# Kernel tuning notes

Hardware: AMD Instinct MI355X
Metric: run time of the kernel (lower is better)

The kernel has to match this reference:

```python
import jax, jax.numpy as jnp
import numpy as np

B, S, E, H = 2, 2048, 4096, 32
D = E // H  # head_dim = 128
MAX_SEQ = 2048


def precompute_freqs(dim, end, theta=10000.0):
    # Faithful to the torch source, including its operator precedence:
    # freqs = 1.0 / (theta ** arange(0, dim, 2)[:dim//2].float() / dim)
    # i.e. 1.0 / ((theta ** exps) / dim); overflows to inf in fp32 -> freq 0.
    exps = jnp.arange(0, dim, 2, dtype=jnp.float32)[: dim // 2]
    freqs = 1.0 / (jnp.power(jnp.float32(theta), exps) / jnp.float32(dim))
    t = jnp.arange(end, dtype=jnp.float32)
    f = jnp.outer(t, freqs)  # [end, dim//2]
    return jnp.cos(f), jnp.sin(f)


def apply_rope(x, cos, sin, pos):
    # x: [B,H,S,D]; cos/sin: [max_seq, dim//2]; pos: [B,S]
    c = cos[pos][:, None]  # [B,1,S,f]
    s = sin[pos][:, None]
    xr = x.reshape(*x.shape[:-1], -1, 2)  # [B,H,S,D/2,2]
    x1, x2 = xr[..., 0], xr[..., 1]
    if x1.shape[-1] > c.shape[-1]:
        rep = x1.shape[-1] // c.shape[-1]  # repeat_interleave factor
        c = jnp.repeat(c, rep, axis=-1)
        s = jnp.repeat(s, rep, axis=-1)
    out = jnp.stack([x1 * c - x2 * s, x1 * s + x2 * c], axis=-1)
    return out.reshape(x.shape)


def setup_inputs() -> dict:
    key = jax.random.key(0)
    kx, kq, kk, kv, ko = jax.random.split(key, 5)
    x = jax.random.normal(kx, (B, S, E), jnp.float32)
    scale = 0.02
    Wq = jax.random.normal(kq, (E, E), jnp.float32) * scale
    Wk = jax.random.normal(kk, (E, E), jnp.float32) * scale
    Wv = jax.random.normal(kv, (E, E), jnp.float32) * scale
    Wo = jax.random.normal(ko, (E, E), jnp.float32) * scale
    z = jnp.zeros((E,), jnp.float32)
    return {"x": x, "Wq": Wq, "bq": z, "Wk": Wk, "bk": z, "Wv": Wv, "bv": z, "Wo": Wo, "bo": z}


def reference(x, Wq, bq, Wk, bk, Wv, bv, Wo, bo):
    cos, sin = precompute_freqs(H, MAX_SEQ)  # note: dim = n_heads, as in source
    pos = jnp.broadcast_to(jnp.arange(S)[None, :], (B, S))  # no offset, S <= max
    # QKV projections (torch Linear: x @ W.T + b)
    q = (x @ Wq.T + bq).reshape(B, S, H, D).transpose(0, 2, 1, 3)  # [B,H,S,D]
    k = (x @ Wk.T + bk).reshape(B, S, H, D).transpose(0, 2, 1, 3)
    v = (x @ Wv.T + bv).reshape(B, S, H, D).transpose(0, 2, 1, 3)
    q = apply_rope(q, cos, sin, pos)
    k = apply_rope(k, cos, sin, pos)
    # SDPA with mask=None (non-causal, full attention)
    scores = jnp.einsum("bhqd,bhkd->bhqk", q, k) / np.float32(np.sqrt(D))
    att = jax.nn.softmax(scores, axis=-1)
    out = jnp.einsum("bhqk,bhkd->bhqd", att, v)
    out = out.transpose(0, 2, 1, 3).reshape(B, S, E)
    return out @ Wo.T + bo
```

## Files before the change

kernel.cpp:

```cpp
#include <hip/hip_runtime.h>
#include <math.h>

typedef _Float16 half8 __attribute__((ext_vector_type(8)));
typedef float f32x4 __attribute__((ext_vector_type(4)));

struct FreqT { float f[16]; };

__device__ __forceinline__ f32x4 mfma16(half8 a, half8 b, f32x4 c) {
  return __builtin_amdgcn_mfma_f32_16x16x32_f16(a, b, c, 0, 0, 0);
}

__device__ __forceinline__ void gload_lds16(const void* g, void* l) {
  __builtin_amdgcn_global_load_lds(
      (const __attribute__((address_space(1))) void*)g,
      (__attribute__((address_space(3))) void*)l, 16, 0, 0);
}

#define S_BARRIER() __builtin_amdgcn_s_barrier()
#define WAIT_LGKM0() asm volatile("s_waitcnt lgkmcnt(0)" ::: "memory")
#define WAIT_VM8() asm volatile("s_waitcnt vmcnt(8)" ::: "memory")
#define WAIT_VM0() asm volatile("s_waitcnt vmcnt(0)" ::: "memory")

__global__ __launch_bounds__(256)
void cast_f32_f16(const float* __restrict__ in, _Float16* __restrict__ out, long n8) {
  long i = (long)blockIdx.x * blockDim.x + threadIdx.x;
  if (i >= n8) return;
  float4 a = ((const float4*)in)[2 * i];
  float4 b = ((const float4*)in)[2 * i + 1];
  half8 v;
  v[0] = (_Float16)a.x; v[1] = (_Float16)a.y; v[2] = (_Float16)a.z; v[3] = (_Float16)a.w;
  v[4] = (_Float16)b.x; v[5] = (_Float16)b.y; v[6] = (_Float16)b.z; v[7] = (_Float16)b.w;
  ((half8*)out)[i] = v;
}

#define GBM 256
#define GBN 256
#define GBK 64

template <typename OutT>
__global__ __launch_bounds__(512, 2)
void gemm256(const _Float16* __restrict__ A, const _Float16* __restrict__ W,
             const float* __restrict__ bias, OutT* __restrict__ C,
             int M, int N, int K) {
  __shared__ __align__(16) _Float16 lds[4][GBM * GBK];

  int nwg = gridDim.x;
  int bid = blockIdx.x;
  int cpx = nwg >> 3;
  int swz = (bid & 7) * cpx + (bid >> 3);
  int ntn = N / GBN;
  int m0 = (swz / ntn) * GBM, n0 = (swz % ntn) * GBN;

  int tid = threadIdx.x, lane = tid & 63, w = tid >> 6;
  int wm = w >> 2, wn = w & 3;
  int g = lane >> 4, lc = lane & 15;

  int r8 = w * 8 + (lane >> 3);
  int cs = (((lane & 7) ^ (lane >> 3)) << 3);
  const _Float16* gA = A + (size_t)(m0 + r8) * K + cs;
  const _Float16* gB = W + (size_t)(n0 + r8) * K + cs;

#define STAGE(bi, k0) do {                                            \
    _Float16* la_ = &lds[(bi) * 2][0] + w * 512;                      \
    _Float16* lb_ = &lds[(bi) * 2 + 1][0] + w * 512;                  \
    _Pragma("unroll")                                                 \
    for (int i_ = 0; i_ < 4; ++i_) {                                  \
      gload_lds16(gA + (size_t)(i_ * 64) * K + (k0), la_ + i_ * 4096);\
      gload_lds16(gB + (size_t)(i_ * 64) * K + (k0), lb_ + i_ * 4096);\
    } } while (0)

  int aOff[8], bOff[4];
#pragma unroll
  for (int mf = 0; mf < 8; ++mf) aOff[mf] = (wm * 128 + mf * 16 + lc) * 64;
#pragma unroll
  for (int nf = 0; nf < 4; ++nf) bOff[nf] = (wn * 64 + nf * 16 + lc) * 64;
  int co0 = (((0 * 4 + g) ^ (lc & 7)) << 3);
  int co1 = (((1 * 4 + g) ^ (lc & 7)) << 3);

  half8 a0[8], a1[8], b0[4], b1[4];
  f32x4 acc[8][4] = {};

#define LOAD_SET0(bi) do {                                            \
    const _Float16* lA_ = &lds[(bi) * 2][0];                          \
    const _Float16* lB_ = &lds[(bi) * 2 + 1][0];                      \
    _Pragma("unroll")                                                 \
    for (int mf = 0; mf < 4; ++mf) {                                  \
      a0[mf * 2 + 0] = *(const half8*)&lA_[aOff[mf] + co0];           \
      a0[mf * 2 + 1] = *(const half8*)&lA_[aOff[mf] + co1];           \
    }                                                                 \
    _Pragma("unroll")                                                 \
    for (int nf = 0; nf < 2; ++nf) {                                  \
      b0[nf * 2 + 0] = *(const half8*)&lB_[bOff[nf] + co0];           \
      b0[nf * 2 + 1] = *(const half8*)&lB_[bOff[nf] + co1];           \
    } } while (0)

#define LOAD_SET1(bi) do {                                            \
    const _Float16* lA_ = &lds[(bi) * 2][0];                          \
    const _Float16* lB_ = &lds[(bi) * 2 + 1][0];                      \
    _Pragma("unroll")                                                 \
    for (int mf = 0; mf < 4; ++mf) {                                  \
      a1[mf * 2 + 0] = *(const half8*)&lA_[aOff[mf + 4] + co0];       \
      a1[mf * 2 + 1] = *(const half8*)&lA_[aOff[mf + 4] + co1];       \
    }                                                                 \
    _Pragma("unroll")                                                 \
    for (int nf = 0; nf < 2; ++nf) {                                  \
      b1[nf * 2 + 0] = *(const half8*)&lB_[bOff[nf + 2] + co0];       \
      b1[nf * 2 + 1] = *(const half8*)&lB_[bOff[nf + 2] + co1];       \
    } } while (0)

#define MFMA_Q(mq, nq, ar, br) do {                                   \
    __builtin_amdgcn_s_setprio(1);                                    \
    _Pragma("unroll")                                                 \
    for (int mf = 0; mf < 4; ++mf)                                    \
      _Pragma("unroll")                                               \
      for (int nf = 0; nf < 2; ++nf)                                  \
        _Pragma("unroll")                                             \
        for (int kk = 0; kk < 2; ++kk)                                \
          acc[(mq) * 4 + mf][(nq) * 2 + nf] =                         \
              mfma16(ar[mf * 2 + kk], br[nf * 2 + kk],                \
                     acc[(mq) * 4 + mf][(nq) * 2 + nf]);              \
    __builtin_amdgcn_s_setprio(0); } while (0)

  const int NT = K >> 6;

  STAGE(0, 0);
  STAGE(1, GBK);
  WAIT_VM8();
  S_BARRIER();
  LOAD_SET0(0);

  for (int t = 0; t < NT - 2; ++t) {
    int cur = t & 1;
    LOAD_SET1(cur);
    MFMA_Q(0, 0, a0, b0);
    MFMA_Q(0, 1, a0, b1);
    WAIT_LGKM0();
    S_BARRIER();
    STAGE(cur, (t + 2) << 6);
    MFMA_Q(1, 1, a1, b1);
    MFMA_Q(1, 0, a1, b0);
    WAIT_VM8();
    S_BARRIER();
    LOAD_SET0(cur ^ 1);
  }
  {
    int cur = (NT - 2) & 1;
    LOAD_SET1(cur);
    MFMA_Q(0, 0, a0, b0);
    MFMA_Q(0, 1, a0, b1);
    MFMA_Q(1, 1, a1, b1);
    MFMA_Q(1, 0, a1, b0);
    WAIT_VM0();
    S_BARRIER();
    LOAD_SET0(cur ^ 1);
  }
  {
    int cur = (NT - 1) & 1;
    LOAD_SET1(cur);
    MFMA_Q(0, 0, a0, b0);
    MFMA_Q(0, 1, a0, b1);
    MFMA_Q(1, 1, a1, b1);
    MFMA_Q(1, 0, a1, b0);
  }

  int crow = m0 + wm * 128 + g * 4;
  int ccol = n0 + wn * 64 + lc;
#pragma unroll
  for (int nf = 0; nf < 4; ++nf) {
    float bv = bias[ccol + nf * 16];
#pragma unroll
    for (int mf = 0; mf < 8; ++mf)
#pragma unroll
      for (int j = 0; j < 4; ++j)
        C[(size_t)(crow + mf * 16 + j) * N + ccol + nf * 16] =
            (OutT)(acc[mf][nf][j] + bv);
  }
#undef STAGE
#undef LOAD_SET0
#undef LOAD_SET1
#undef MFMA_Q
}

__global__ __launch_bounds__(256)
void rope_kernel(_Float16* __restrict__ x, FreqT ft, int Sn, int E, long n8) {
  long i = (long)blockIdx.x * blockDim.x + threadIdx.x;
  if (i >= n8) return;
  int epr = E / 8;
  int e8 = (int)(i % epr);
  int s = (int)((i / epr) % Sn);
  int fj = e8 & 15;
  float fr = ft.f[fj];
  float ang = (float)s * fr;
  float sv, cv;
  sincosf(ang, &sv, &cv);
  half8 v = ((const half8*)x)[i];
  half8 o;
#pragma unroll
  for (int p = 0; p < 4; ++p) {
    float x1 = (float)v[2 * p], x2 = (float)v[2 * p + 1];
    o[2 * p] = (_Float16)(x1 * cv - x2 * sv);
    o[2 * p + 1] = (_Float16)(x1 * sv + x2 * cv);
  }
  ((half8*)x)[i] = o;
}

#define QB 128
#define KB 64

__global__ __launch_bounds__(256)
void flash_attn(const _Float16* __restrict__ qg, const _Float16* __restrict__ kg,
                const _Float16* __restrict__ vg, _Float16* __restrict__ og,
                int Bn, int Hn, int Sn) {
  const int D = 128;
  const int E = Hn * D;

  __shared__ _Float16 Ksh[KB * 128];
  __shared__ _Float16 Vsh[128 * 64];
  __shared__ _Float16 Psh[4 * 32 * 64];

  int qtiles = Sn / QB;
  int bid = blockIdx.x;
  int bh = bid / qtiles, qt = bid % qtiles;
  int b = bh / Hn, h = bh % Hn;

  int tid = threadIdx.x, lane = tid & 63, w = tid >> 6;
  int g = lane >> 4, lc = lane & 15;
  int lc7 = lc & 7;

  const size_t headoff = ((size_t)b * Sn) * E + (size_t)h * D;
  const _Float16* qp = qg + headoff;
  const _Float16* kp = kg + headoff;
  const _Float16* vp = vg + headoff;

  int q0 = qt * QB + w * 32;
  half8 aq[2][4];
#pragma unroll
  for (int mf = 0; mf < 2; ++mf)
#pragma unroll
    for (int kf = 0; kf < 4; ++kf)
      aq[mf][kf] = *(const half8*)(qp + (size_t)(q0 + mf * 16 + lc) * E + kf * 32 + g * 8);

  float mrun[2][4], lpart[2][4];
  f32x4 o[2][8] = {};
#pragma unroll
  for (int mf = 0; mf < 2; ++mf)
#pragma unroll
    for (int j = 0; j < 4; ++j) { mrun[mf][j] = -1e30f; lpart[mf][j] = 0.f; }

  const float scale = 0.08838834764831845f;

  int krow = 4 * w + (lane >> 4);
  int kcol = ((lane & 15) ^ (krow & 7)) * 8;
  const _Float16* gK = kp + (size_t)krow * E + kcol;
  _Float16* lK = Ksh + w * 512;

  half8 vreg[4];
#pragma unroll
  for (int p = 0; p < 4; ++p)
    vreg[p] = *(const half8*)(vp + (size_t)lane * E + p * 32 + w * 8);

  int kvlo = lane & 7, kvhi = lane >> 3;
  _Float16* Pw = Psh + w * 2048;

  const int NT = Sn / KB;
  for (int kt = 0; kt < NT; ++kt) {
    __syncthreads();
#pragma unroll
    for (int i = 0; i < 4; ++i)
      gload_lds16(gK + (size_t)(kt * KB + 16 * i) * E, lK + i * 2048);
#pragma unroll
    for (int p = 0; p < 4; ++p) {
      int d0 = p * 32 + w * 8;
#pragma unroll
      for (int i = 0; i < 8; ++i)
        Vsh[(d0 + i) * 64 + (kvlo | (((kvhi ^ i) & 7) << 3))] = vreg[p][i];
    }
    __syncthreads();

    f32x4 s[2][4] = {};
    __builtin_amdgcn_s_setprio(1);
#pragma unroll
    for (int kf = 0; kf < 4; ++kf) {
      half8 bk[4];
#pragma unroll
      for (int nf = 0; nf < 4; ++nf)
        bk[nf] = *(const half8*)&Ksh[(nf * 16 + lc) * 128 + (((kf * 4 + g) ^ lc7) << 3)];
#pragma unroll
      for (int mf = 0; mf < 2; ++mf)
#pragma unroll
        for (int nf = 0; nf < 4; ++nf)
          s[mf][nf] = mfma16(aq[mf][kf], bk[nf], s[mf][nf]);
    }
    __builtin_amdgcn_s_setprio(0);

#pragma unroll
    for (int mf = 0; mf < 2; ++mf) {
      f32x4 mx = s[mf][0];
#pragma unroll
      for (int nf = 1; nf < 4; ++nf)
#pragma unroll
        for (int j = 0; j < 4; ++j) mx[j] = fmaxf(mx[j], s[mf][nf][j]);
#pragma unroll
      for (int d = 1; d < 16; d <<= 1)
#pragma unroll
        for (int j = 0; j < 4; ++j) mx[j] = fmaxf(mx[j], __shfl_xor(mx[j], d));
      bool need = false;
#pragma unroll
      for (int j = 0; j < 4; ++j) need |= (mx[j] * scale > mrun[mf][j] + 8.f);
      if (__any(need)) {
#pragma unroll
        for (int j = 0; j < 4; ++j) {
          float mnew = fmaxf(mrun[mf][j], mx[j] * scale);
          float r = __expf(mrun[mf][j] - mnew);
          mrun[mf][j] = mnew;
          lpart[mf][j] *= r;
#pragma unroll
          for (int df = 0; df < 8; ++df) o[mf][df][j] *= r;
        }
      }
#pragma unroll
      for (int nf = 0; nf < 4; ++nf) {
        int colbase = nf * 16 + lc;
        int chi = colbase >> 3, clo = colbase & 7;
#pragma unroll
        for (int j = 0; j < 4; ++j) {
          float p = __expf(s[mf][nf][j] * scale - mrun[mf][j]);
          lpart[mf][j] += p;
          int row = mf * 16 + g * 4 + j;
          Pw[row * 64 + (clo | (((chi ^ (row & 7)) & 7) << 3))] = (_Float16)p;
        }
      }
    }

    if (kt + 1 < NT) {
#pragma unroll
      for (int p = 0; p < 4; ++p)
        vreg[p] = *(const half8*)(vp + (size_t)((kt + 1) * KB + lane) * E + p * 32 + w * 8);
    }

    __builtin_amdgcn_s_setprio(1);
#pragma unroll
    for (int kk = 0; kk < 2; ++kk) {
      half8 ap0 = *(const half8*)&Pw[lc * 64 + (((kk * 4 + g) ^ lc7) << 3)];
      half8 ap1 = *(const half8*)&Pw[(16 + lc) * 64 + (((kk * 4 + g) ^ lc7) << 3)];
#pragma unroll
      for (int df = 0; df < 8; ++df) {
        half8 bv = *(const half8*)&Vsh[(df * 16 + lc) * 64 + (((kk * 4 + g) ^ lc7) << 3)];
        o[0][df] = mfma16(ap0, bv, o[0][df]);
        o[1][df] = mfma16(ap1, bv, o[1][df]);
      }
    }
    __builtin_amdgcn_s_setprio(0);
  }

  _Float16* op = og + headoff;
#pragma unroll
  for (int mf = 0; mf < 2; ++mf) {
#pragma unroll
    for (int j = 0; j < 4; ++j) {
      float l = lpart[mf][j];
#pragma unroll
      for (int d = 1; d < 16; d <<= 1) l += __shfl_xor(l, d);
      float inv = 1.0f / l;
      int row = q0 + mf * 16 + g * 4 + j;
#pragma unroll
      for (int df = 0; df < 8; ++df)
        op[(size_t)row * E + df * 16 + lc] = (_Float16)(o[mf][df][j] * inv);
    }
  }
}

extern "C" void kernel_launch(void* const* d_in, const int* in_sizes, int n_in,
                              void* d_out, int out_size, void* d_ws, size_t ws_size,
                              hipStream_t stream) {
  const float* x  = (const float*)d_in[0];
  const float* Wq = (const float*)d_in[1];
  const float* bq = (const float*)d_in[2];
  const float* Wk = (const float*)d_in[3];
  const float* bk = (const float*)d_in[4];
  const float* Wv = (const float*)d_in[5];
  const float* bv = (const float*)d_in[6];
  const float* Wo = (const float*)d_in[7];
  const float* bo = (const float*)d_in[8];

  const int E = in_sizes[2];
  const int M = in_sizes[0] / E;
  const int S = 2048;
  const int Bb = M / S;
  const int H = 32;

  _Float16* xh = (_Float16*)d_ws;
  _Float16* wh = xh + (size_t)M * E;
  _Float16* qh = wh + (size_t)E * E;
  _Float16* kh = qh + (size_t)M * E;
  _Float16* vh = kh + (size_t)M * E;
  _Float16* oh = xh;

  FreqT ft;
  for (int j = 0; j < 16; ++j) {
    float pf = (float)pow(10000.0, (double)(2 * j));
    ft.f[j] = 1.0f / (pf / 32.0f);
  }

  long nx8 = (long)M * E / 8;
  long nw8 = (long)E * E / 8;
  dim3 blk(256);
  int cb_x = (int)((nx8 + 255) / 256);
  int cb_w = (int)((nw8 + 255) / 256);
  int gemm_grid = (M / GBM) * (E / GBN);

  cast_f32_f16<<<cb_x, blk, 0, stream>>>(x, xh, nx8);

  cast_f32_f16<<<cb_w, blk, 0, stream>>>(Wq, wh, nw8);
  gemm256<_Float16><<<gemm_grid, 512, 0, stream>>>(xh, wh, bq, qh, M, E, E);
  cast_f32_f16<<<cb_w, blk, 0, stream>>>(Wk, wh, nw8);
  gemm256<_Float16><<<gemm_grid, 512, 0, stream>>>(xh, wh, bk, kh, M, E, E);
  cast_f32_f16<<<cb_w, blk, 0, stream>>>(Wv, wh, nw8);
  gemm256<_Float16><<<gemm_grid, 512, 0, stream>>>(xh, wh, bv, vh, M, E, E);

  rope_kernel<<<cb_x, blk, 0, stream>>>(qh, ft, S, E, nx8);
  rope_kernel<<<cb_x, blk, 0, stream>>>(kh, ft, S, E, nx8);

  flash_attn<<<Bb * H * (S / QB), blk, 0, stream>>>(qh, kh, vh, oh, Bb, H, S);

  cast_f32_f16<<<cb_w, blk, 0, stream>>>(Wo, wh, nw8);
  gemm256<float><<<gemm_grid, 512, 0, stream>>>(oh, wh, bo, (float*)d_out, M, E, E);
}
```

Baseline: 937.0 us.

## Pre-transpose V and double-buffer K/V async loads in flash attention

Adds a transpose_v kernel that writes V as [B,H,D,S] into the weight workspace, so flash attention can stream V tiles straight into LDS with async global-to-LDS loads instead of staging them through registers and scattering them. K is double-buffered across iterations, and the S=K·Q product is computed transposed so each lane holds a single query row. Row max and sum become cheaper cross-lane reductions, and rescale factors are passed through a small LDS array. The cost is an extra kernel launch plus one extra read and write of V, more LDS, and a launch-bounds hint for two blocks per CU.

Result: faster. 772.0 us (-17.6%).

```diff
diff --git a/kernel.cpp b/kernel.cpp
--- a/kernel.cpp
+++ b/kernel.cpp
@@ -2,6 +2,7 @@
 #include <math.h>
 
 typedef _Float16 half8 __attribute__((ext_vector_type(8)));
+typedef _Float16 half4 __attribute__((ext_vector_type(4)));
 typedef float f32x4 __attribute__((ext_vector_type(4)));
 
 struct FreqT { float f[16]; };
@@ -19,6 +20,7 @@
 #define S_BARRIER() __builtin_amdgcn_s_barrier()
 #define WAIT_LGKM0() asm volatile("s_waitcnt lgkmcnt(0)" ::: "memory")
 #define WAIT_VM8() asm volatile("s_waitcnt vmcnt(8)" ::: "memory")
+#define WAIT_VM4() asm volatile("s_waitcnt vmcnt(4)" ::: "memory")
 #define WAIT_VM0() asm volatile("s_waitcnt vmcnt(0)" ::: "memory")
 
 __global__ __launch_bounds__(256)
@@ -155,8 +157,7 @@
     LOAD_SET0(cur ^ 1);
   }
   {
-    int cur = (NT - 1) & 1;
-    LOAD_SET1(cur);
+    LOAD_SET1((NT - 1) & 1);
     MFMA_Q(0, 0, a0, b0);
     MFMA_Q(0, 1, a0, b1);
     MFMA_Q(1, 1, a1, b1);
@@ -204,19 +205,58 @@
   ((half8*)x)[i] = o;
 }
 
+__global__ __launch_bounds__(256)
+void transpose_v(const _Float16* __restrict__ v, _Float16* __restrict__ vt,
+                 int Hn, int Sn) {
+  const int D = 128;
+  const int E = Hn * D;
+  __shared__ _Float16 t[64][130];
+  int spb = Sn / 64;
+  int bid = blockIdx.x;
+  int s0 = (bid % spb) * 64;
+  int bh = bid / spb;
+  int b = bh / Hn, h = bh % Hn;
+  int tid = threadIdx.x;
+  int r = tid >> 2, dc = (tid & 3) * 32;
+  const _Float16* src = v + (size_t)(b * Sn + s0 + r) * E + h * D + dc;
+#pragma unroll
+  for (int i = 0; i < 4; ++i) {
+    half8 x = *(const half8*)(src + i * 8);
+#pragma unroll
+    for (int k = 0; k < 4; ++k) {
+      _Float16 a0 = x[2 * k], a1 = x[2 * k + 1];
+      t[r][dc + i * 8 + 2 * k] = a0;
+      t[r][dc + i * 8 + 2 * k + 1] = a1;
+    }
+  }
+  __syncthreads();
+  int d = tid >> 1, sh = (tid & 1) * 32;
+  half8 ov[4];
+#pragma unroll
+  for (int c = 0; c < 4; ++c)
+#pragma unroll
+    for (int j = 0; j < 8; ++j)
+      ov[c][j] = t[sh + c * 8 + j][d];
+  _Float16* dst = vt + ((size_t)bh * D + d) * Sn + s0 + sh;
+#pragma unroll
+  for (int c = 0; c < 4; ++c)
+    *(half8*)(dst + c * 8) = ov[c];
+}
+
 #define QB 128
 #define KB 64
 
-__global__ __launch_bounds__(256)
+__global__ __launch_bounds__(256, 2)
 void flash_attn(const _Float16* __restrict__ qg, const _Float16* __restrict__ kg,
-                const _Float16* __restrict__ vg, _Float16* __restrict__ og,
+                const _Float16* __restrict__ vt, _Float16* __restrict__ og,
                 int Bn, int Hn, int Sn) {
   const int D = 128;
   const int E = Hn * D;
 
-  __shared__ _Float16 Ksh[KB * 128];
-  __shared__ _Float16 Vsh[128 * 64];
-  __shared__ _Float16 Psh[4 * 32 * 64];
+  __shared__ _Float16 Ksh[2][KB * 128];
+  __shared__ _Float16 Vsh[D * KB];
+  __shared__ _Float16 Psh[4][32 * 64];
+  __shared__ float sm[4][32];
 
   int qtiles = Sn / QB;
   int bid = blockIdx.x;
@@ -230,7 +270,7 @@
   const size_t headoff = ((size_t)b * Sn) * E + (size_t)h * D;
   const _Float16* qp = qg + headoff;
   const _Float16* kp = kg + headoff;
-  const _Float16* vp = vg + headoff;
+  const _Float16* vtp = vt + (size_t)(b * Hn + h) * D * Sn;
 
   int q0 = qt * QB + w * 32;
   half8 aq[2][4];
@@ -240,132 +280,155 @@
     for (int kf = 0; kf < 4; ++kf)
       aq[mf][kf] = *(const half8*)(qp + (size_t)(q0 + mf * 16 + lc) * E + kf * 32 + g * 8);
 
-  float mrun[2][4], lpart[2][4];
+  float mrun[2] = {-1e30f, -1e30f}, lpart[2] = {0.f, 0.f};
   f32x4 o[2][8] = {};
-#pragma unroll
-  for (int mf = 0; mf < 2; ++mf)
-#pragma unroll
-    for (int j = 0; j < 4; ++j) { mrun[mf][j] = -1e30f; lpart[mf][j] = 0.f; }
 
   const float scale = 0.08838834764831845f;
 
   int krow = 4 * w + (lane >> 4);
   int kcol = ((lane & 15) ^ (krow & 7)) * 8;
   const _Float16* gK = kp + (size_t)krow * E + kcol;
-  _Float16* lK = Ksh + w * 512;
-
-  half8 vreg[4];
-#pragma unroll
-  for (int p = 0; p < 4; ++p)
-    vreg[p] = *(const half8*)(vp + (size_t)lane * E + p * 32 + w * 8);
-
-  int kvlo = lane & 7, kvhi = lane >> 3;
-  _Float16* Pw = Psh + w * 2048;
+  int vrow = w * 32 + (lane >> 3);
+  int vcol = ((lane & 7) ^ (vrow & 7)) * 8;
+  const _Float16* gV = vtp + (size_t)vrow * Sn + vcol;
+
+  _Float16* Pw = Psh[w];
+  float* smw = sm[w];
 
   const int NT = Sn / KB;
-  for (int kt = 0; kt < NT; ++kt) {
-    __syncthreads();
+
+  {
+    _Float16* lK = Ksh[0] + w * 512;
 #pragma unroll
     for (int i = 0; i < 4; ++i)
-      gload_lds16(gK + (size_t)(kt * KB + 16 * i) * E, lK + i * 2048);
-#pragma unroll
-    for (int p = 0; p < 4; ++p) {
-      int d0 = p * 32 + w * 8;
-#pragma unroll
-      for (int i = 0; i < 8; ++i)
-        Vsh[(d0 + i) * 64 + (kvlo | (((kvhi ^ i) & 7) << 3))] = vreg[p][i];
-    }
-    __syncthreads();
-
-    f32x4 s[2][4] = {};
+      gload_lds16(gK + (size_t)(16 * i) * E, lK + i * 2048);
+  }
+  WAIT_VM0();
+  S_BARRIER();
+
+  for (int t = 0; t < NT; ++t) {
+    int c = t & 1;
+    {
+      _Float16* lV = Vsh + w * 2048;
+#pragma unroll
+      for (int p = 0; p < 4; ++p)
+        gload_lds16(gV + (size_t)(p * 8) * Sn + t * KB, lV + p * 512);
+    }
+    if (t + 1 < NT) {
+      _Float16* lK = Ksh[c ^ 1] + w * 512;
+#pragma unroll
+      for (int i = 0; i < 4; ++i)
+        gload_lds16(gK + (size_t)((t + 1) * KB + 16 * i) * E, lK + i * 2048);
+    }
+
+    f32x4 st[2][4] = {};
+    {
+      const _Float16* Kc = Ksh[c];
+      __builtin_amdgcn_s_setprio(1);
+#pragma unroll
+      for (int kf = 0; kf < 4; ++kf) {
+        half8 bk[4];
+#pragma unroll
+        for (int nf = 0; nf < 4; ++nf)
+          bk[nf] = *(const half8*)&Kc[(nf * 16 + lc) * 128 + (((kf * 4 + g) ^ lc7) << 3)];
+#pragma unroll
+        for (int nf = 0; nf < 4; ++nf)
+#pragma unroll
+          for (int mf = 0; mf < 2; ++mf)
+            st[mf][nf] = mfma16(bk[nf], aq[mf][kf], st[mf][nf]);
+      }
+      __builtin_amdgcn_s_setprio(0);
+    }
+
+    bool resc[2];
+#pragma unroll
+    for (int mf = 0; mf < 2; ++mf) {
+      f32x4 m4 = st[mf][0];
+#pragma unroll
+      for (int nf = 1; nf < 4; ++nf)
+#pragma unroll
+        for (int j = 0; j < 4; ++j) m4[j] = fmaxf(m4[j], st[mf][nf][j]);
+      float mx = fmaxf(fmaxf(m4[0], m4[1]), fmaxf(m4[2], m4[3]));
+      mx = fmaxf(mx, __shfl_xor(mx, 16));
+      mx = fmaxf(mx, __shfl_xor(mx, 32));
+      mx *= scale;
+      resc[mf] = __any(mx > mrun[mf] + 8.f);
+      if (resc[mf]) {
+        float mnew = fmaxf(mrun[mf], mx);
+        float r = __expf(mrun[mf] - mnew);
+        mrun[mf] = mnew;
+        lpart[mf] *= r;
+        if (g == 0) smw[mf * 16 + lc] = r;
+      }
+    }
+#pragma unroll
+    for (int mf = 0; mf < 2; ++mf)
+      if (resc[mf]) {
+        f32x4 rv = *(const f32x4*)&smw[mf * 16 + g * 4];
+#pragma unroll
+        for (int df = 0; df < 8; ++df)
+#pragma unroll
+          for (int j = 0; j < 4; ++j) o[mf][df][j] *= rv[j];
+      }
+#pragma unroll
+    for (int mf = 0; mf < 2; ++mf) {
+      int rowoff = (mf * 16 + lc) * 64;
+#pragma unroll
+      for (int nf = 0; nf < 4; ++nf) {
+        half4 p4;
+        float ls = 0.f;
+#pragma unroll
+        for (int j = 0; j < 4; ++j) {
+          float p = __expf(st[mf][nf][j] * scale - mrun[mf]);
+          ls += p;
+          p4[j] = (_Float16)p;
+        }
+        lpart[mf] += ls;
+        *(half4*)&Pw[rowoff + ((((nf * 2 + (g >> 1)) ^ lc7) << 3) + ((g & 1) << 2))] = p4;
+      }
+    }
+
+    if (t + 1 < NT) { WAIT_VM4(); } else { WAIT_VM0(); }
+    S_BARRIER();
+
     __builtin_amdgcn_s_setprio(1);
 #pragma unroll
-    for (int kf = 0; kf < 4; ++kf) {
-      half8 bk[4];
-#pragma unroll
-      for (int nf = 0; nf < 4; ++nf)
-        bk[nf] = *(const half8*)&Ksh[(nf * 16 + lc) * 128 + (((kf * 4 + g) ^ lc7) << 3)];
-#pragma unroll
-      for (int mf = 0; mf < 2; ++mf)
-#pragma unroll
-        for (int nf = 0; nf < 4; ++nf)
-          s[mf][nf] = mfma16(aq[mf][kf], bk[nf], s[mf][nf]);
-    }
-    __builtin_amdgcn_s_setprio(0);
-
-#pragma unroll
-    for (int mf = 0; mf < 2; ++mf) {
-      f32x4 mx = s[mf][0];
-#pragma unroll
-      for (int nf = 1; nf < 4; ++nf)
-#pragma unroll
-        for (int j = 0; j < 4; ++j) mx[j] = fmaxf(mx[j], s[mf][nf][j]);
-#pragma unroll
-      for (int d = 1; d < 16; d <<= 1)
-#pragma unroll
-        for (int j = 0; j < 4; ++j) mx[j] = fmaxf(mx[j], __shfl_xor(mx[j], d));
-      bool need = false;
-#pragma unroll
-      for (int j = 0; j < 4; ++j) need |= (mx[j] * scale > mrun[mf][j] + 8.f);
-      if (__any(need)) {
-#pragma unroll
-        for (int j = 0; j < 4; ++j) {
-          float mnew = fmaxf(mrun[mf][j], mx[j] * scale);
-          float r = __expf(mrun[mf][j] - mnew);
-          mrun[mf][j] = mnew;
-          lpart[mf][j] *= r;
-#pragma unroll
-          for (int df = 0; df < 8; ++df) o[mf][df][j] *= r;
-        }
-      }
-#pragma unroll
-      for (int nf = 0; nf < 4; ++nf) {
-        int colbase = nf * 16 + lc;
-        int chi = colbase >> 3, clo = colbase & 7;
-#pragma unroll
-        for (int j = 0; j < 4; ++j) {
-          float p = __expf(s[mf][nf][j] * scale - mrun[mf][j]);
-          lpart[mf][j] += p;
-          int row = mf * 16 + g * 4 + j;
-          Pw[row * 64 + (clo | (((chi ^ (row & 7)) & 7) << 3))] = (_Float16)p;
-        }
-      }
-    }
-
-    if (kt + 1 < NT) {
-#pragma unroll
-      for (int p = 0; p < 4; ++p)
-        vreg[p] = *(const half8*)(vp + (size_t)((kt + 1) * KB + lane) * E + p * 32 + w * 8);
-    }
-
-    __builtin_amdgcn_s_setprio(1);
-#pragma unroll
     for (int kk = 0; kk < 2; ++kk) {
-      half8 ap0 = *(const half8*)&Pw[lc * 64 + (((kk * 4 + g) ^ lc7) << 3)];
-      half8 ap1 = *(const half8*)&Pw[(16 + lc) * 64 + (((kk * 4 + g) ^ lc7) << 3)];
+      int csw = ((kk * 4 + g) ^ lc7) << 3;
+      half8 ap0 = *(const half8*)&Pw[lc * 64 + csw];
+      half8 ap1 = *(const half8*)&Pw[(16 + lc) * 64 + csw];
 #pragma unroll
       for (int df = 0; df < 8; ++df) {
-        half8 bv = *(const half8*)&Vsh[(df * 16 + lc) * 64 + (((kk * 4 + g) ^ lc7) << 3)];
+        half8 bv = *(const half8*)&Vsh[(df * 16 + lc) * 64 + csw];
         o[0][df] = mfma16(ap0, bv, o[0][df]);
         o[1][df] = mfma16(ap1, bv, o[1][df]);
       }
     }
     __builtin_amdgcn_s_setprio(0);
-  }
-
+
+    if (t + 1 < NT) {
+      WAIT_VM0();
+      S_BARRIER();
+    }
+  }
+
+#pragma unroll
+  for (int mf = 0; mf < 2; ++mf) {
+    float l = lpart[mf];
+    l += __shfl_xor(l, 16);
+    l += __shfl_xor(l, 32);
+    if (g == 0) smw[mf * 16 + lc] = 1.0f / l;
+  }
   _Float16* op = og + headoff;
 #pragma unroll
   for (int mf = 0; mf < 2; ++mf) {
+    f32x4 li = *(const f32x4*)&smw[mf * 16 + g * 4];
 #pragma unroll
     for (int j = 0; j < 4; ++j) {
-      float l = lpart[mf][j];
-#pragma unroll
-      for (int d = 1; d < 16; d <<= 1) l += __shfl_xor(l, d);
-      float inv = 1.0f / l;
       int row = q0 + mf * 16 + g * 4 + j;
 #pragma unroll
       for (int df = 0; df < 8; ++df)
-        op[(size_t)row * E + df * 16 + lc] = (_Float16)(o[mf][df][j] * inv);
+        op[(size_t)row * E + df * 16 + lc] = (_Float16)(o[mf][df][j] * li[j]);
     }
   }
 }
@@ -395,6 +458,7 @@
   _Float16* kh = qh + (size_t)M * E;
   _Float16* vh = kh + (size_t)M * E;
   _Float16* oh = xh;
+  _Float16* vtb = wh;
 
   FreqT ft;
   for (int j = 0; j < 16; ++j) {
@@ -421,7 +485,9 @@
   rope_kernel<<<cb_x, blk, 0, stream>>>(qh, ft, S, E, nx8);
   rope_kernel<<<cb_x, blk, 0, stream>>>(kh, ft, S, E, nx8);
 
-  flash_attn<<<Bb * H * (S / QB), blk, 0, stream>>>(qh, kh, vh, oh, Bb, H, S);
+  transpose_v<<<Bb * H * (S / 64), blk, 0, stream>>>(vh, vtb, H, S);
+
+  flash_attn<<<Bb * H * (S / QB), blk, 0, stream>>>(qh, kh, vtb, oh, Bb, H, S);
 
   cast_f32_f16<<<cb_w, blk, 0, stream>>>(Wo, wh, nw8);
   gemm256<float><<<gemm_grid, 512, 0, stream>>>(oh, wh, bo, (float*)d_out, M, E, E);
```
